# Performance work log

Measured on AMD Instinct MI355X. Metric: run time of the kernel, lower is better.

## Reference

```python
import jax, jax.numpy as jnp
import numpy as np

N_QUBITS = 10
STATE_DIM = 2 ** N_QUBITS
BATCH = 32768


def setup_inputs() -> dict:
    key = jax.random.key(0)
    k1, k2 = jax.random.split(key)
    base_state = jax.random.normal(k1, (BATCH, STATE_DIM), dtype=jnp.float32)
    # nn.Parameter(torch.rand(n_qubits) * 2*pi)
    gate_params = jax.random.uniform(k2, (N_QUBITS,), dtype=jnp.float32) * 2.0 * np.pi
    return {"base_state": base_state, "gate_params": gate_params}


def _simulate(base_state, gate_params):
    n = gate_params.shape[0]
    B = base_state.shape[0]
    # AmplitudeEmbedding with normalize=True: L2-normalize, promote to complex.
    norm = jnp.linalg.norm(base_state, axis=1, keepdims=True)
    state = (base_state / norm).astype(jnp.complex64)
    # PennyLane wire 0 is the most-significant bit -> axis order matches reshape.
    state = state.reshape((B,) + (2,) * n)

    # RY(theta_i) on wire i: [[cos, -sin], [sin, cos]] with half-angles.
    half = gate_params.astype(jnp.float32) / 2.0
    c, s = jnp.cos(half), jnp.sin(half)
    for i in range(n):
        U = jnp.stack([jnp.stack([c[i], -s[i]]), jnp.stack([s[i], c[i]])]).astype(jnp.complex64)
        st = jnp.moveaxis(state, i + 1, -1)          # (..., 2) on wire i
        st = st @ U.T                                 # new[j] = sum_k U[j,k] old[k]
        state = jnp.moveaxis(st, -1, i + 1)

    # CNOT chain: control i, target i+1 (flip target slice where control = 1).
    for i in range(n - 1):
        st = jnp.moveaxis(state, (i + 1, i + 2), (-2, -1))  # (..., ctrl, tgt)
        st = jnp.stack([st[..., 0, :], st[..., 1, ::-1]], axis=-2)
        state = jnp.moveaxis(st, (-2, -1), (i + 1, i + 2))

    # Pauli expectation values per wire, in order [X_i, Y_i, Z_i].
    meas = []
    for i in range(n):
        st = jnp.moveaxis(state, i + 1, 1)            # (B, 2, rest...)
        s0 = st[:, 0].reshape(B, -1)
        s1 = st[:, 1].reshape(B, -1)
        cross = jnp.sum(jnp.conj(s0) * s1, axis=1)    # <psi0|psi1> partial
        X = 2.0 * jnp.real(cross)
        Y = 2.0 * jnp.imag(cross)
        Z = jnp.sum(jnp.real(s0 * jnp.conj(s0)) - jnp.real(s1 * jnp.conj(s1)), axis=1)
        meas += [X, Y, Z]
    return jnp.stack(meas, axis=1).astype(jnp.float32)  # (B, 3*n)


def reference(base_state, gate_params):
    return _simulate(base_state, gate_params)
```

## Files before the change

### kernel.cpp

```cpp
#include <hip/hip_runtime.h>


#define NQ 10
#define DIM 1024

__device__ __forceinline__ int swz(int u) {
    return u ^ ((u >> 3) & 7) ^ ((u >> 6) & 7);
}

template <int CTRL, int RMASK>
__device__ __forceinline__ float dpp_mov(float x) {
    return __int_as_float(
        __builtin_amdgcn_update_dpp(0, __float_as_int(x), CTRL, RMASK, 0xF, true));
}

__device__ __forceinline__ float red32(float x) {
    x += dpp_mov<0x111, 0xF>(x);
    x += dpp_mov<0x112, 0xF>(x);
    x += dpp_mov<0x114, 0xF>(x);
    x += dpp_mov<0x118, 0xF>(x);
    x += dpp_mov<0x142, 0xA>(x);
    return x;
}

template <int MASK>
__device__ __forceinline__ void gate(float (&v)[32], float cc, float ss) {
#pragma unroll
    for (int j = 0; j < 32; ++j) {
        if ((j & MASK) == 0) {
            const float a0 = v[j], a1 = v[j | MASK];
            v[j]        = cc * a0 - ss * a1;
            v[j | MASK] = ss * a0 + cc * a1;
        }
    }
}

template <int MASK, int COND>
__device__ __forceinline__ float xsum(const float (&v)[32]) {
    float a = 0.f;
#pragma unroll
    for (int j = 0; j < 32; ++j)
        if ((j & COND) == 0) a = fmaf(v[j], v[j ^ MASK], a);
    return a;
}

__device__ __forceinline__ float f4alt(const float* a) {
    const float b0 = a[0] - a[1],   b1 = a[2] - a[3];
    const float b2 = a[4] - a[5],   b3 = a[6] - a[7];
    const float b4 = a[8] - a[9],   b5 = a[10] - a[11];
    const float b6 = a[12] - a[13], b7 = a[14] - a[15];
    const float c0 = b0 - b1, c1 = b2 - b3, c2 = b4 - b5, c3 = b6 - b7;
    return (c0 - c1) - (c2 - c3);
}

extern "C" __global__ void __launch_bounds__(256, 4)
qsim_kernel(const float* __restrict__ base, const float* __restrict__ prm,
            float* __restrict__ out) {
    __shared__ float lds[4][2048];

    const int tid  = threadIdx.x;
    const int wid  = tid >> 6;
    const int lane = tid & 63;
    const int sub  = lane & 31;
    const int st   = lane >> 5;
    const int sid  = blockIdx.x * 8 + wid * 2 + st;
    float* slab = lds[wid];

    float c[NQ], s[NQ];
#pragma unroll
    for (int i = 0; i < NQ; ++i) {
        const float h = 0.5f * prm[i];
        s[i] = __sinf(h);
        c[i] = __cosf(h);
    }

    float v[32];
    const float4* row = reinterpret_cast<const float4*>(base + (size_t)sid * DIM);
#pragma unroll
    for (int q = 0; q < 8; ++q) {
        const float4 t = row[(sub << 3) | q];
        v[4 * q + 0] = t.x; v[4 * q + 1] = t.y;
        v[4 * q + 2] = t.z; v[4 * q + 3] = t.w;
    }
    float n2 = 0.f;
#pragma unroll
    for (int j = 0; j < 32; ++j) n2 = fmaf(v[j], v[j], n2);

    gate<1>(v, c[9], s[9]);
    gate<2>(v, c[8], s[8]);
    gate<4>(v, c[7], s[7]);
    gate<8>(v, c[6], s[6]);
    gate<16>(v, c[5], s[5]);

#pragma unroll
    for (int q = 0; q < 8; ++q) {
        const int u = (st << 8) | (sub << 3) | q;
        reinterpret_cast<float4*>(slab)[swz(u)] =
            make_float4(v[4 * q], v[4 * q + 1], v[4 * q + 2], v[4 * q + 3]);
    }
    asm volatile("s_waitcnt lgkmcnt(0)" ::: "memory");
#pragma unroll
    for (int q = 0; q < 8; ++q) {
        const int u = (st << 8) | (sub & 7) | (q << 3) | ((sub >> 3) << 6);
        const float4 t = reinterpret_cast<const float4*>(slab)[swz(u)];
        v[4 * q + 0] = t.x; v[4 * q + 1] = t.y;
        v[4 * q + 2] = t.z; v[4 * q + 3] = t.w;
    }

    gate<4>(v, c[4], s[4]);
    gate<8>(v, c[3], s[3]);
    gate<16>(v, c[2], s[2]);

#pragma unroll
    for (int q = 0; q < 8; ++q) {
        const int u = (st << 8) | (sub & 7) | (q << 3) | ((sub >> 3) << 6);
        reinterpret_cast<float4*>(slab)[swz(u)] =
            make_float4(v[4 * q], v[4 * q + 1], v[4 * q + 2], v[4 * q + 3]);
    }
    asm volatile("s_waitcnt lgkmcnt(0)" ::: "memory");
#pragma unroll
    for (int t = 0; t < 8; ++t) {
        const int u = (st << 8) | (t & 1) | (sub << 1) |
                      (((t >> 1) & 1) << 6) | ((t >> 2) << 7);
        const float4 r = reinterpret_cast<const float4*>(slab)[swz(u)];
        v[4 * t + 0] = r.x; v[4 * t + 1] = r.y;
        v[4 * t + 2] = r.z; v[4 * t + 3] = r.w;
    }

    gate<8>(v, c[1], s[1]);
    gate<16>(v, c[0], s[0]);

    float xa[NQ], za[NQ];
    xa[9] = xsum<1, 1>(v);
    xa[8] = xsum<3, 2>(v);
    xa[7] = xsum<6, 4>(v);
    xa[0] = xsum<24, 16>(v);

    {
        float A1[16], D1[16];
#pragma unroll
        for (int k = 0; k < 16; ++k) {
            const float s0 = v[2 * k] * v[2 * k];
            const float s1 = v[2 * k + 1] * v[2 * k + 1];
            A1[k] = s0 + s1;
            D1[k] = s0 - s1;
        }
        const float I0 = f4alt(D1);
        const float I1 = f4alt(A1);
        float A2[8];
#pragma unroll
        for (int k = 0; k < 8; ++k) A2[k] = A1[2 * k] + A1[2 * k + 1];
        const float I2 = ((A2[0] - A2[1]) - (A2[2] - A2[3])) -
                         ((A2[4] - A2[5]) - (A2[6] - A2[7]));
        float A3[4];
#pragma unroll
        for (int k = 0; k < 4; ++k) A3[k] = A2[2 * k] + A2[2 * k + 1];
        const float I8 = (A3[0] - A3[1]) - (A3[2] - A3[3]);
        const float I9 = (A3[0] + A3[1]) - (A3[2] + A3[3]);

        const float sg0 = (__popc(sub) & 1) ? -1.f : 1.f;
        const float sg1 = (__popc(sub >> 1) & 1) ? -1.f : 1.f;
        const float sg2 = (__popc(sub >> 2) & 1) ? -1.f : 1.f;
        const float sg3 = (__popc(sub >> 3) & 1) ? -1.f : 1.f;
        const float sg4 = (__popc(sub >> 4) & 1) ? -1.f : 1.f;

        za[0] = I9;
        za[1] = I8;
        za[2] = sg4 * I8;
        za[3] = sg3 * I8;
        za[4] = sg2 * I8;
        za[5] = sg1 * I8;
        za[6] = sg0 * I8;
        za[7] = sg0 * I2;
        za[8] = sg0 * I1;
        za[9] = sg0 * I0;
    }

#pragma unroll
    for (int t = 0; t < 8; ++t) {
        const int u = (st << 8) | (t & 1) | (sub << 1) |
                      (((t >> 1) & 1) << 6) | ((t >> 2) << 7);
        reinterpret_cast<float4*>(slab)[swz(u)] =
            make_float4(v[4 * t], v[4 * t + 1], v[4 * t + 2], v[4 * t + 3]);
    }
    asm volatile("s_waitcnt lgkmcnt(0)" ::: "memory");
#pragma unroll
    for (int p = 0; p < 16; ++p) {
        const int u  = (st << 8) | ((sub >> 1) & 7) | (p << 3) | ((sub >> 4) << 7);
        const int fi = (swz(u) << 2) | ((sub & 1) << 1);
        const float2 r = *reinterpret_cast<const float2*>(slab + fi);
        v[2 * p] = r.x; v[2 * p + 1] = r.y;
    }

    xa[3] = xsum<6, 4>(v);
    xa[2] = xsum<12, 8>(v);
    xa[1] = xsum<24, 16>(v);

#pragma unroll
    for (int p = 0; p < 16; ++p) {
        const int u  = (st << 8) | ((sub >> 1) & 7) | (p << 3) | ((sub >> 4) << 7);
        const int fi = (swz(u) << 2) | ((sub & 1) << 1);
        *reinterpret_cast<float2*>(slab + fi) = make_float2(v[2 * p], v[2 * p + 1]);
    }
    asm volatile("s_waitcnt lgkmcnt(0)" ::: "memory");
#pragma unroll
    for (int p = 0; p < 16; ++p) {
        const int u  = (st << 8) | p | ((sub >> 1) << 4);
        const int fi = (swz(u) << 2) | ((sub & 1) << 1);
        const float2 r = *reinterpret_cast<const float2*>(slab + fi);
        v[2 * p] = r.x; v[2 * p + 1] = r.y;
    }

    xa[6] = xsum<6, 4>(v);
    xa[5] = xsum<12, 8>(v);
    xa[4] = xsum<24, 16>(v);

    n2 = red32(n2);
#pragma unroll
    for (int w = 0; w < NQ; ++w) {
        xa[w] = red32(xa[w]);
        za[w] = red32(za[w]);
    }

    if (sub == 31) {
        const float inv = 1.0f / n2;
        float* o = out + (size_t)sid * (3 * NQ);
#pragma unroll
        for (int w = 0; w < NQ; ++w) {
            o[3 * w + 0] = 2.0f * xa[w] * inv;
            o[3 * w + 1] = 0.0f;
            o[3 * w + 2] = za[w] * inv;
        }
    }
}

extern "C" void kernel_launch(void* const* d_in, const int* in_sizes, int n_in,
                              void* d_out, int out_size, void* d_ws, size_t ws_size,
                              hipStream_t stream) {
    const float* base = (const float*)d_in[0];
    const float* prm  = (const float*)d_in[1];
    float* out        = (float*)d_out;
    const int nstates = in_sizes[0] / DIM;
    const int blocks  = nstates / 8;
    qsim_kernel<<<dim3(blocks), dim3(256), 0, stream>>>(base, prm, out);
}
```

Baseline: 189.9 us.

## Remap qubit-to-lane layout to cut LDS transposes and use DPP for cross-lane sums

Global loads now use a strided lane layout, so each thread gets a different qubit assignment and five gates can be applied before the first shared-memory exchange. The number of LDS round trips drops from four to two, using padded slabs with XOR-offset indexing instead of the swizzle function. Two of the X-expectation partial sums are computed with DPP lane swizzles rather than another transpose. The norm is taken from the Z sum, since RY gates preserve it, which removes the separate norm accumulation. The cost is more complex index arithmetic, scalar LDS reads, and a higher risk of subtle correctness errors.

```diff
diff --git a/kernel.cpp b/kernel.cpp
--- a/kernel.cpp
+++ b/kernel.cpp
@@ -3,10 +3,7 @@
 
 #define NQ 10
 #define DIM 1024
-
-__device__ __forceinline__ int swz(int u) {
-    return u ^ ((u >> 3) & 7) ^ ((u >> 6) & 7);
-}
+#define SLABF 1028
 
 template <int CTRL, int RMASK>
 __device__ __forceinline__ float dpp_mov(float x) {
@@ -56,7 +53,7 @@
 extern "C" __global__ void __launch_bounds__(256, 4)
 qsim_kernel(const float* __restrict__ base, const float* __restrict__ prm,
             float* __restrict__ out) {
-    __shared__ float lds[4][2048];
+    __shared__ float lds[4][2 * SLABF];
 
     const int tid  = threadIdx.x;
     const int wid  = tid >> 6;
@@ -64,7 +61,13 @@
     const int sub  = lane & 31;
     const int st   = lane >> 5;
     const int sid  = blockIdx.x * 8 + wid * 2 + st;
-    float* slab = lds[wid];
+    float* slab  = lds[wid];
+    float4* slab4 = reinterpret_cast<float4*>(slab);
+    const int stF = st * SLABF;
+    const int stU = st * (SLABF / 4);
+
+    const int b0 = sub & 1, b1 = (sub >> 1) & 1, b2 = (sub >> 2) & 1,
+              b3 = (sub >> 3) & 1, b4 = (sub >> 4) & 1;
 
     float c[NQ], s[NQ];
 #pragma unroll
@@ -75,147 +78,136 @@
     }
 
     float v[32];
-    const float4* row = reinterpret_cast<const float4*>(base + (size_t)sid * DIM);
+    const float4* row4 = reinterpret_cast<const float4*>(base + (size_t)sid * DIM);
 #pragma unroll
     for (int q = 0; q < 8; ++q) {
-        const float4 t = row[(sub << 3) | q];
+        const float4 t = row4[(q << 5) | sub];
         v[4 * q + 0] = t.x; v[4 * q + 1] = t.y;
         v[4 * q + 2] = t.z; v[4 * q + 3] = t.w;
     }
-    float n2 = 0.f;
-#pragma unroll
-    for (int j = 0; j < 32; ++j) n2 = fmaf(v[j], v[j], n2);
 
     gate<1>(v, c[9], s[9]);
     gate<2>(v, c[8], s[8]);
-    gate<4>(v, c[7], s[7]);
-    gate<8>(v, c[6], s[6]);
-    gate<16>(v, c[5], s[5]);
-
-#pragma unroll
-    for (int q = 0; q < 8; ++q) {
-        const int u = (st << 8) | (sub << 3) | q;
-        reinterpret_cast<float4*>(slab)[swz(u)] =
-            make_float4(v[4 * q], v[4 * q + 1], v[4 * q + 2], v[4 * q + 3]);
-    }
-    asm volatile("s_waitcnt lgkmcnt(0)" ::: "memory");
-#pragma unroll
-    for (int q = 0; q < 8; ++q) {
-        const int u = (st << 8) | (sub & 7) | (q << 3) | ((sub >> 3) << 6);
-        const float4 t = reinterpret_cast<const float4*>(slab)[swz(u)];
-        v[4 * q + 0] = t.x; v[4 * q + 1] = t.y;
-        v[4 * q + 2] = t.z; v[4 * q + 3] = t.w;
-    }
-
-    gate<4>(v, c[4], s[4]);
-    gate<8>(v, c[3], s[3]);
-    gate<16>(v, c[2], s[2]);
-
-#pragma unroll
-    for (int q = 0; q < 8; ++q) {
-        const int u = (st << 8) | (sub & 7) | (q << 3) | ((sub >> 3) << 6);
-        reinterpret_cast<float4*>(slab)[swz(u)] =
-            make_float4(v[4 * q], v[4 * q + 1], v[4 * q + 2], v[4 * q + 3]);
-    }
-    asm volatile("s_waitcnt lgkmcnt(0)" ::: "memory");
-#pragma unroll
-    for (int t = 0; t < 8; ++t) {
-        const int u = (st << 8) | (t & 1) | (sub << 1) |
-                      (((t >> 1) & 1) << 6) | ((t >> 2) << 7);
-        const float4 r = reinterpret_cast<const float4*>(slab)[swz(u)];
-        v[4 * t + 0] = r.x; v[4 * t + 1] = r.y;
-        v[4 * t + 2] = r.z; v[4 * t + 3] = r.w;
-    }
-
+    gate<4>(v, c[2], s[2]);
     gate<8>(v, c[1], s[1]);
     gate<16>(v, c[0], s[0]);
 
+#pragma unroll
+    for (int q = 0; q < 8; ++q) {
+        slab4[stU + (q << 5) + (sub ^ ((q >> 1) << 1))] =
+            make_float4(v[4 * q], v[4 * q + 1], v[4 * q + 2], v[4 * q + 3]);
+    }
+    asm volatile("s_waitcnt lgkmcnt(0)" ::: "memory");
+    {
+        const int rb = stF + ((sub >> 2) << 7) + (sub & 3);
+        const int xj = (sub >> 3) << 1;
+#pragma unroll
+        for (int p = 0; p < 16; ++p) {
+            const int a = rb + (((2 * p) ^ xj) << 2);
+            v[2 * p]     = slab[a];
+            v[2 * p + 1] = slab[a + 4];
+        }
+    }
+
+    gate<1>(v, c[7], s[7]);
+    gate<2>(v, c[6], s[6]);
+    gate<4>(v, c[5], s[5]);
+    gate<8>(v, c[4], s[4]);
+    gate<16>(v, c[3], s[3]);
+
     float xa[NQ], za[NQ];
+    xa[6] = xsum<3, 2>(v);
+    xa[5] = xsum<6, 4>(v);
+    xa[4] = xsum<12, 8>(v);
+    xa[3] = xsum<24, 16>(v);
+
+    {
+        float f8 = 0.f, f7 = 0.f;
+#pragma unroll
+        for (int j = 0; j < 32; ++j)
+            f8 = fmaf(v[j], dpp_mov<0x1B, 0xF>(v[j]), f8);
+#pragma unroll
+        for (int j = 0; j < 32; ++j)
+            f7 = fmaf(v[j], dpp_mov<0x4E, 0xF>(v[j ^ 1]), f7);
+        xa[8] = 0.5f * f8;
+        xa[7] = 0.5f * f7;
+    }
+
+    {
+        float A1[16], D1[16];
+#pragma unroll
+        for (int k = 0; k < 16; ++k) {
+            const float s0q = v[2 * k] * v[2 * k];
+            const float s1q = v[2 * k + 1] * v[2 * k + 1];
+            A1[k] = s0q + s1q;
+            D1[k] = s0q - s1q;
+        }
+        const float S31 = f4alt(D1);
+        const float S30 = f4alt(A1);
+        float A2[8];
+#pragma unroll
+        for (int k = 0; k < 8; ++k) A2[k] = A1[2 * k] + A1[2 * k + 1];
+        const float S28 = ((A2[0] - A2[1]) - (A2[2] - A2[3])) -
+                          ((A2[4] - A2[5]) - (A2[6] - A2[7]));
+        float A3[4];
+#pragma unroll
+        for (int k = 0; k < 4; ++k) A3[k] = A2[2 * k] + A2[2 * k + 1];
+        const float S24 = (A3[0] - A3[1]) - (A3[2] - A3[3]);
+        const float S16 = (A3[0] + A3[1]) - (A3[2] + A3[3]);
+        const float S0  = (A3[0] + A3[1]) + (A3[2] + A3[3]);
+
+        const float sgA = (__popc(sub >> 2) & 1) ? -1.f : 1.f;
+        const float sg9 = b4 ? -1.f : 1.f;
+        const float sg89 = (__popc(sub >> 3) & 1) ? -1.f : 1.f;
+        const float sg1A = (__popc(sub >> 1) & 1) ? -1.f : 1.f;
+        const float sg0A = (__popc(sub) & 1) ? -1.f : 1.f;
+
+        za[0] = sg9 * S0;
+        za[1] = sg89 * S0;
+        za[2] = sgA * S0;
+        za[3] = sgA * S16;
+        za[4] = sgA * S24;
+        za[5] = sgA * S28;
+        za[6] = sgA * S30;
+        za[7] = sgA * S31;
+        za[8] = sg1A * S31;
+        za[9] = sg0A * S31;
+        xa[0] = S0;
+    }
+    float S0v;
+    {
+        const float sgA = (__popc(sub >> 2) & 1) ? -1.f : 1.f;
+        S0v = sgA * za[2];
+    }
+
+#pragma unroll
+    for (int p = 0; p < 8; ++p) {
+        const int uh = b0 | (b1 << 1) | ((b2 ^ (p & 1)) << 2) | (p << 3) |
+                       (b3 << 6) | (b4 << 7);
+        slab4[stU + uh] = make_float4(v[4 * p], v[4 * p + 1], v[4 * p + 2], v[4 * p + 3]);
+    }
+    asm volatile("s_waitcnt lgkmcnt(0)" ::: "memory");
+    {
+        const int low = b1 | (b2 << 1);
+#pragma unroll
+        for (int p = 0; p < 16; ++p) {
+            const int j  = 2 * p;
+            const int j1 = (j >> 1) & 1, j2 = (j >> 2) & 1,
+                      j3 = (j >> 3) & 1, j4 = (j >> 4) & 1;
+            const int uh = (b0 << 1) | ((j2 ^ b3) << 2) | (b3 << 3) | (b4 << 4) |
+                           (j1 << 5) | (j3 << 6) | (j4 << 7);
+            const int a = stF + (uh << 2) + low;
+            v[j]     = slab[a];
+            v[j + 1] = slab[a + 4];
+        }
+    }
+
     xa[9] = xsum<1, 1>(v);
-    xa[8] = xsum<3, 2>(v);
-    xa[7] = xsum<6, 4>(v);
+    xa[2] = xsum<6, 4>(v);
+    xa[1] = xsum<12, 8>(v);
     xa[0] = xsum<24, 16>(v);
 
-    {
-        float A1[16], D1[16];
-#pragma unroll
-        for (int k = 0; k < 16; ++k) {
-            const float s0 = v[2 * k] * v[2 * k];
-            const float s1 = v[2 * k + 1] * v[2 * k + 1];
-            A1[k] = s0 + s1;
-            D1[k] = s0 - s1;
-        }
-        const float I0 = f4alt(D1);
-        const float I1 = f4alt(A1);
-        float A2[8];
-#pragma unroll
-        for (int k = 0; k < 8; ++k) A2[k] = A1[2 * k] + A1[2 * k + 1];
-        const float I2 = ((A2[0] - A2[1]) - (A2[2] - A2[3])) -
-                         ((A2[4] - A2[5]) - (A2[6] - A2[7]));
-        float A3[4];
-#pragma unroll
-        for (int k = 0; k < 4; ++k) A3[k] = A2[2 * k] + A2[2 * k + 1];
-        const float I8 = (A3[0] - A3[1]) - (A3[2] - A3[3]);
-        const float I9 = (A3[0] + A3[1]) - (A3[2] + A3[3]);
-
-        const float sg0 = (__popc(sub) & 1) ? -1.f : 1.f;
-        const float sg1 = (__popc(sub >> 1) & 1) ? -1.f : 1.f;
-        const float sg2 = (__popc(sub >> 2) & 1) ? -1.f : 1.f;
-        const float sg3 = (__popc(sub >> 3) & 1) ? -1.f : 1.f;
-        const float sg4 = (__popc(sub >> 4) & 1) ? -1.f : 1.f;
-
-        za[0] = I9;
-        za[1] = I8;
-        za[2] = sg4 * I8;
-        za[3] = sg3 * I8;
-        za[4] = sg2 * I8;
-        za[5] = sg1 * I8;
-        za[6] = sg0 * I8;
-        za[7] = sg0 * I2;
-        za[8] = sg0 * I1;
-        za[9] = sg0 * I0;
-    }
-
-#pragma unroll
-    for (int t = 0; t < 8; ++t) {
-        const int u = (st << 8) | (t & 1) | (sub << 1) |
-                      (((t >> 1) & 1) << 6) | ((t >> 2) << 7);
-        reinterpret_cast<float4*>(slab)[swz(u)] =
-            make_float4(v[4 * t], v[4 * t + 1], v[4 * t + 2], v[4 * t + 3]);
-    }
-    asm volatile("s_waitcnt lgkmcnt(0)" ::: "memory");
-#pragma unroll
-    for (int p = 0; p < 16; ++p) {
-        const int u  = (st << 8) | ((sub >> 1) & 7) | (p << 3) | ((sub >> 4) << 7);
-        const int fi = (swz(u) << 2) | ((sub & 1) << 1);
-        const float2 r = *reinterpret_cast<const float2*>(slab + fi);
-        v[2 * p] = r.x; v[2 * p + 1] = r.y;
-    }
-
-    xa[3] = xsum<6, 4>(v);
-    xa[2] = xsum<12, 8>(v);
-    xa[1] = xsum<24, 16>(v);
-
-#pragma unroll
-    for (int p = 0; p < 16; ++p) {
-        const int u  = (st << 8) | ((sub >> 1) & 7) | (p << 3) | ((sub >> 4) << 7);
-        const int fi = (swz(u) << 2) | ((sub & 1) << 1);
-        *reinterpret_cast<float2*>(slab + fi) = make_float2(v[2 * p], v[2 * p + 1]);
-    }
-    asm volatile("s_waitcnt lgkmcnt(0)" ::: "memory");
-#pragma unroll
-    for (int p = 0; p < 16; ++p) {
-        const int u  = (st << 8) | p | ((sub >> 1) << 4);
-        const int fi = (swz(u) << 2) | ((sub & 1) << 1);
-        const float2 r = *reinterpret_cast<const float2*>(slab + fi);
-        v[2 * p] = r.x; v[2 * p + 1] = r.y;
-    }
-
-    xa[6] = xsum<6, 4>(v);
-    xa[5] = xsum<12, 8>(v);
-    xa[4] = xsum<24, 16>(v);
-
-    n2 = red32(n2);
+    float n2 = red32(S0v);
 #pragma unroll
     for (int w = 0; w < NQ; ++w) {
         xa[w] = red32(xa[w]);
```

After: 190.6 us. No clear change (+0.3%).
